# Performance work log

Measured on AMD Instinct MI355X. Metric: run time of the kernel, lower is better.

Reference implementation:

```python
import jax, jax.numpy as jnp
import numpy as np

N_USER, N_TX, E = 50000, 50000, 600000
D_USER, D_TX, D_ALIGN, HID, OUT = 128, 64, 128, 256, 128


def setup_inputs() -> dict:
    key = jax.random.key(0)
    ks = jax.random.split(key, 16)
    s = 0.05
    return {
        "x_user": jax.random.normal(ks[0], (N_USER, D_USER), jnp.float32),
        "x_tx": jax.random.normal(ks[1], (N_TX, D_TX), jnp.float32),
        "edge_user_tx": jax.random.randint(ks[2], (2, E), 0, N_USER),
        "edge_tx_user": jax.random.randint(ks[3], (2, E), 0, N_TX),
        "W_align_user": jax.random.normal(ks[4], (D_USER, D_ALIGN), jnp.float32) * s,
        "b_align_user": jnp.zeros((D_ALIGN,), jnp.float32),
        "W_align_tx": jax.random.normal(ks[5], (D_TX, D_ALIGN), jnp.float32) * s,
        "b_align_tx": jnp.zeros((D_ALIGN,), jnp.float32),
        "eps_ut": jnp.zeros((), jnp.float32),
        "eps_tu": jnp.zeros((), jnp.float32),
        "W1_ut": jax.random.normal(ks[6], (D_TX + D_ALIGN, HID), jnp.float32) * s,
        "b1_ut": jnp.zeros((HID,), jnp.float32),
        "W2_ut": jax.random.normal(ks[7], (HID, OUT), jnp.float32) * s,
        "b2_ut": jnp.zeros((OUT,), jnp.float32),
        "W1_tu": jax.random.normal(ks[8], (D_USER + D_ALIGN, HID), jnp.float32) * s,
        "b1_tu": jnp.zeros((HID,), jnp.float32),
        "W2_tu": jax.random.normal(ks[9], (HID, OUT), jnp.float32) * s,
        "b2_tu": jnp.zeros((OUT,), jnp.float32),
    }


def _mlp(h, W1, b1, W2, b2):
    return jnp.maximum(h @ W1 + b1, 0.0) @ W2 + b2


def _hexgin_conv(x_src, x_dst, edge_index, W_a, b_a, eps, W1, b1, W2, b2):
    # align src features, gather along edges, scatter-sum into dst nodes
    a_src = x_src @ W_a + b_a                       # [N_src, D_ALIGN]
    msgs = a_src[edge_index[0]]                     # [E, D_ALIGN] gather
    agg = jax.ops.segment_sum(msgs, edge_index[1], num_segments=x_dst.shape[0])
    h = jnp.concatenate([(1.0 + eps) * x_dst, agg], axis=1)
    return _mlp(h, W1, b1, W2, b2)


def reference(x_user, x_tx, edge_user_tx, edge_tx_user,
              W_align_user, b_align_user, W_align_tx, b_align_tx,
              eps_ut, eps_tu,
              W1_ut, b1_ut, W2_ut, b2_ut,
              W1_tu, b1_tu, W2_tu, b2_tu):
    # relation (user, makes, tx): updates tx nodes
    out_tx = _hexgin_conv(x_user, x_tx, edge_user_tx,
                          W_align_user, b_align_user, eps_ut,
                          W1_ut, b1_ut, W2_ut, b2_ut)
    # relation (tx, to, user): updates user nodes
    out_user = _hexgin_conv(x_tx, x_user, edge_tx_user,
                            W_align_tx, b_align_tx, eps_tu,
                            W1_tu, b1_tu, W2_tu, b2_tu)
    # HeteroConv aggr='sum': single relation per target, so plain outputs
    return out_user, out_tx
```

## Files before the change

kernel.cpp:

```cpp
#include <hip/hip_runtime.h>
#include <hip/hip_bf16.h>


#define D_USER 128
#define D_TX 64
#define D_ALIGN 128
#define HID 256
#define OUT_D 128
#define NNODE 50000
#define BI 32
#define MAXSLOT 62

typedef __attribute__((ext_vector_type(8))) short short8;
typedef __attribute__((ext_vector_type(4))) float f32x4;
typedef unsigned short ush;

__device__ __forceinline__ ush f2bf(float f) {
    union { float f; unsigned u; } v; v.f = f;
    unsigned u = v.u + 0x7fffu + ((v.u >> 16) & 1u);
    return (ush)(u >> 16);
}
__device__ __forceinline__ float2 bfu2f(unsigned u) {
    union { unsigned u; float f; } a, b;
    a.u = (u & 0xffffu) << 16;
    b.u = u & 0xffff0000u;
    return make_float2(a.f, b.f);
}
__device__ __forceinline__ unsigned f2bfu(float2 v) {
    return (unsigned)f2bf(v.x) | ((unsigned)f2bf(v.y) << 16);
}
__device__ __forceinline__ uint4 scale_bf8(uint4 v, float e) {
    unsigned* w = (unsigned*)&v;
    #pragma unroll
    for (int t = 0; t < 4; ++t) {
        float2 f = bfu2f(w[t]);
        w[t] = f2bfu(make_float2(f.x * e, f.y * e));
    }
    return v;
}


__device__ __forceinline__ void dev_fill(const int* __restrict__ e, int E, int i,
                                         int* __restrict__ pad, int dbase)
{
    int d = dbase + e[E + i];
    int s = e[i];
    int pos = atomicAdd(&pad[(size_t)d * BI], 1);
    if (pos < MAXSLOT)
        ((ush*)pad)[(size_t)d * (2 * BI) + 2 + pos] = (ush)s;
}

__device__ __forceinline__ void dev_prep(int b, int tid,
    const float* __restrict__ xu, ush* __restrict__ xbu,
    const float* __restrict__ xt, ush* __restrict__ xbt, int n8u, int n8t,
    const float* __restrict__ Wa_u, const float* __restrict__ ba_u,
    const float* __restrict__ W1_ut,
    const float* __restrict__ Wa_t, const float* __restrict__ ba_t,
    const float* __restrict__ W1_tu,
    const float* __restrict__ W2_ut, const float* __restrict__ W2_tu,
    ush* __restrict__ Bt1a, float* __restrict__ bfv1,
    ush* __restrict__ Bt1b, float* __restrict__ bfv2,
    ush* __restrict__ Bt2a, ush* __restrict__ Bt2b, int gb)
{
    if (b < gb) {
        int i = b * 256 + tid;
        const float* x; ush* xb; int j;
        if (i < n8u) { x = xu; xb = xbu; j = i; }
        else if (i < n8u + n8t) { x = xt; xb = xbt; j = i - n8u; }
        else return;
        const float4 a = *reinterpret_cast<const float4*>(&x[(size_t)j * 8]);
        const float4 c = *reinterpret_cast<const float4*>(&x[(size_t)j * 8 + 4]);
        ush o[8];
        o[0] = f2bf(a.x); o[1] = f2bf(a.y); o[2] = f2bf(a.z); o[3] = f2bf(a.w);
        o[4] = f2bf(c.x); o[5] = f2bf(c.y); o[6] = f2bf(c.z); o[7] = f2bf(c.w);
        *reinterpret_cast<uint4*>(&xb[(size_t)j * 8]) = *reinterpret_cast<uint4*>(o);
        return;
    }
    int idx = (b - gb) * 256 + tid;
    const int KT = 192;
    const int SEG1 = HID * (KT + 1);
    const int SEG2 = OUT_D * HID;
    if (idx < 2 * SEG1) {
        bool r2 = idx >= SEG1;
        int id = r2 ? idx - SEG1 : idx;
        const float* Wa = r2 ? Wa_t : Wa_u;
        const float* ba = r2 ? ba_t : ba_u;
        const float* W1 = r2 ? W1_tu : W1_ut;
        ush* Bt = r2 ? Bt1b : Bt1a;
        float* bfv = r2 ? bfv2 : bfv1;
        const int Dd = r2 ? 128 : 64;
        int c = id & (HID - 1);
        int k = id >> 8;
        const float* w1bot = W1 + (size_t)Dd * HID;
        if (k < Dd) {
            Bt[(size_t)c * KT + k] = f2bf(W1[(size_t)k * HID + c]);
        } else if (k < KT) {
            int ks = k - Dd;
            float acc = 0.f;
            for (int j = 0; j < D_ALIGN; ++j)
                acc += Wa[ks * D_ALIGN + j] * w1bot[(size_t)j * HID + c];
            Bt[(size_t)c * KT + k] = f2bf(acc);
        } else {
            float acc = 0.f;
            for (int j = 0; j < D_ALIGN; ++j)
                acc += ba[j] * w1bot[(size_t)j * HID + c];
            bfv[c] = acc;
        }
    } else if (idx < 2 * SEG1 + 2 * SEG2) {
        int id = idx - 2 * SEG1;
        bool r2 = id >= SEG2;
        if (r2) id -= SEG2;
        const float* W2 = r2 ? W2_tu : W2_ut;
        ush* Bt2 = r2 ? Bt2b : Bt2a;
        int c = id & (OUT_D - 1);
        int k = id >> 7;
        Bt2[(size_t)c * HID + k] = f2bf(W2[(size_t)k * OUT_D + c]);
    }
}

__device__ __forceinline__ int slot_word(const int* blk, int lane)
{
    return ((lane & 31) < 31) ? blk[1 + (lane & 31)] : 0;
}
__device__ __forceinline__ int slot_get(int word, int j)
{
    return (j & 1) ? ((word >> 16) & 0xffff) : (word & 0xffff);
}

__device__ __forceinline__ void dev_agg128(int w, int lane,
    const ush* __restrict__ xbu, const int* __restrict__ pad, ush* __restrict__ Sb1)
{
    const int* blk = pad + (size_t)w * BI;
    const int n = min(blk[0], MAXSLOT);
    const int word = slot_word(blk, lane);
    float2 acc = make_float2(0.f, 0.f);
    int i = 0;
    for (; i + 4 <= n; i += 4) {
        int wa = __shfl(word, i >> 1);
        int wb = __shfl(word, (i >> 1) + 1);
        int s0 = wa & 0xffff, s1 = (wa >> 16) & 0xffff;
        int s2 = wb & 0xffff, s3 = (wb >> 16) & 0xffff;
        unsigned v0 = *reinterpret_cast<const unsigned*>(&xbu[(size_t)s0 * 128 + 2 * lane]);
        unsigned v1 = *reinterpret_cast<const unsigned*>(&xbu[(size_t)s1 * 128 + 2 * lane]);
        unsigned v2 = *reinterpret_cast<const unsigned*>(&xbu[(size_t)s2 * 128 + 2 * lane]);
        unsigned v3 = *reinterpret_cast<const unsigned*>(&xbu[(size_t)s3 * 128 + 2 * lane]);
        float2 f0 = bfu2f(v0), f1 = bfu2f(v1), f2 = bfu2f(v2), f3 = bfu2f(v3);
        acc.x += (f0.x + f1.x) + (f2.x + f3.x);
        acc.y += (f0.y + f1.y) + (f2.y + f3.y);
    }
    for (; i < n; ++i) {
        int ww = __shfl(word, i >> 1);
        int s0 = slot_get(ww, i);
        unsigned v0 = *reinterpret_cast<const unsigned*>(&xbu[(size_t)s0 * 128 + 2 * lane]);
        float2 f0 = bfu2f(v0);
        acc.x += f0.x; acc.y += f0.y;
    }
    *reinterpret_cast<unsigned*>(&Sb1[(size_t)w * 128 + 2 * lane]) = f2bfu(acc);
}

__device__ __forceinline__ void dev_agg64(int w2, int lane,
    const ush* __restrict__ xbt, const int* __restrict__ pad, ush* __restrict__ Sb2)
{
    const int* blk = pad + (size_t)(NNODE + w2) * BI;
    const int n = min(blk[0], MAXSLOT);
    const int word = slot_word(blk, lane);
    const int half = lane >> 5, l2 = lane & 31;
    float2 acc = make_float2(0.f, 0.f);
    int i = 0;
    for (; i + 4 <= n; i += 4) {
        int ja = i + half, jb = i + 2 + half;
        int wa = __shfl(word, ja >> 1);
        int wb = __shfl(word, jb >> 1);
        int s0 = slot_get(wa, ja), s1 = slot_get(wb, jb);
        unsigned v0 = *reinterpret_cast<const unsigned*>(&xbt[(size_t)s0 * 64 + 2 * l2]);
        unsigned v1 = *reinterpret_cast<const unsigned*>(&xbt[(size_t)s1 * 64 + 2 * l2]);
        float2 f0 = bfu2f(v0), f1 = bfu2f(v1);
        acc.x += f0.x + f1.x;
        acc.y += f0.y + f1.y;
    }
    for (; i + 2 <= n; i += 2) {
        int j = i + half;
        int ww = __shfl(word, j >> 1);
        int s0 = slot_get(ww, j);
        unsigned v0 = *reinterpret_cast<const unsigned*>(&xbt[(size_t)s0 * 64 + 2 * l2]);
        float2 f0 = bfu2f(v0);
        acc.x += f0.x; acc.y += f0.y;
    }
    if (i < n && half == 0) {
        int ww = __shfl(word, i >> 1);
        int s0 = slot_get(ww, i);
        unsigned v0 = *reinterpret_cast<const unsigned*>(&xbt[(size_t)s0 * 64 + 2 * l2]);
        float2 f0 = bfu2f(v0);
        acc.x += f0.x; acc.y += f0.y;
    }
    acc.x += __shfl_xor(acc.x, 32);
    acc.y += __shfl_xor(acc.y, 32);
    if (half == 0)
        *reinterpret_cast<unsigned*>(&Sb2[(size_t)w2 * 64 + 2 * l2]) = f2bfu(acc);
}


__global__ __launch_bounds__(256) void kA(
    const int* __restrict__ e_ut, int E, int* __restrict__ pad,
    const float* __restrict__ xu, ush* __restrict__ xbu,
    const float* __restrict__ xt, ush* __restrict__ xbt, int n8u, int n8t,
    const float* __restrict__ Wa_u, const float* __restrict__ ba_u,
    const float* __restrict__ W1_ut,
    const float* __restrict__ Wa_t, const float* __restrict__ ba_t,
    const float* __restrict__ W1_tu,
    const float* __restrict__ W2_ut, const float* __restrict__ W2_tu,
    ush* __restrict__ Bt1a, float* __restrict__ bfv1,
    ush* __restrict__ Bt1b, float* __restrict__ bfv2,
    ush* __restrict__ Bt2a, ush* __restrict__ Bt2b, int gf, int gb)
{
    int b = blockIdx.x, tid = threadIdx.x;
    if (b < gf) {
        int i = b * 256 + tid;
        if (i < E) dev_fill(e_ut, E, i, pad, 0);
    } else {
        dev_prep(b - gf, tid, xu, xbu, xt, xbt, n8u, n8t,
                 Wa_u, ba_u, W1_ut, Wa_t, ba_t, W1_tu, W2_ut, W2_tu,
                 Bt1a, bfv1, Bt1b, bfv2, Bt2a, Bt2b, gb);
    }
}

__global__ __launch_bounds__(256) void kB(
    const int* __restrict__ e_tu, int E, int* __restrict__ pad,
    const ush* __restrict__ xbu, ush* __restrict__ Sb1, int gf)
{
    int b = blockIdx.x, tid = threadIdx.x;
    if (b < gf) {
        int i = b * 256 + tid;
        if (i < E) dev_fill(e_tu, E, i, pad, NNODE);
    } else {
        int w = (b - gf) * 4 + (tid >> 6);
        if (w < NNODE) dev_agg128(w, tid & 63, xbu, pad, Sb1);
    }
}

__global__ __launch_bounds__(256) void kC(
    const ush* __restrict__ xbt, const int* __restrict__ pad, ush* __restrict__ Sb2)
{
    int w2 = blockIdx.x * 4 + (threadIdx.x >> 6);
    if (w2 < NNODE) dev_agg64(w2, threadIdx.x & 63, xbt, pad, Sb2);
}

__global__ __launch_bounds__(256) void mlp1_all(
    const ush* __restrict__ xbt, const ush* __restrict__ xbu,
    const ush* __restrict__ Sb1, const ush* __restrict__ Sb2,
    const ush* __restrict__ Bt1a, const ush* __restrict__ Bt1b,
    const float* __restrict__ bfv1, const float* __restrict__ bfv2,
    const float* __restrict__ b1_ut, const float* __restrict__ b1_tu,
    const int* __restrict__ pad,
    const float* __restrict__ eps_ut, const float* __restrict__ eps_tu,
    ush* __restrict__ hidb1, ush* __restrict__ hidb2, int M, int nb1)
{
    const int KT = 192;
    __shared__ ush As[128 * 40];
    __shared__ ush Bs[128 * 40];
    const int tid = threadIdx.x;
    const bool r2 = (int)blockIdx.y >= nb1;
    const int bm = (r2 ? blockIdx.y - nb1 : blockIdx.y) * 128;
    const int bn = blockIdx.x * 128;
    const ush* xdst = r2 ? xbu : xbt;
    const int Dd = r2 ? 128 : 64;
    const ush* Sb = r2 ? Sb2 : Sb1;
    const int Dsrc = r2 ? 64 : 128;
    const ush* Bt = r2 ? Bt1b : Bt1a;
    const float* bfv = r2 ? bfv2 : bfv1;
    const float* b1 = r2 ? b1_tu : b1_ut;
    const int* dgp = pad + (size_t)(r2 ? NNODE : 0) * BI;
    ush* hidb = r2 ? hidb2 : hidb1;
    const float e = 1.f + (r2 ? eps_tu[0] : eps_ut[0]);

    const int lane = tid & 63, wave = tid >> 6;
    const int wm = wave >> 1, wn = wave & 1;
    const int lo = lane & 15, hi = lane >> 4;

    f32x4 acc[4][4];
    #pragma unroll
    for (int m = 0; m < 4; ++m)
        #pragma unroll
        for (int n = 0; n < 4; ++n)
            acc[m][n] = f32x4{0.f, 0.f, 0.f, 0.f};

    for (int k0 = 0; k0 < KT; k0 += 32) {
        const ush* src = (k0 < Dd) ? xdst : Sb;
        const int ld   = (k0 < Dd) ? Dd : Dsrc;
        const int kb   = (k0 < Dd) ? k0 : k0 - Dd;
        const bool scale = (k0 < Dd);
        #pragma unroll
        for (int q = 0; q < 2; ++q) {
            int idx = tid + 256 * q;
            int r = idx >> 2, c8 = idx & 3;
            int gr = bm + r;
            uint4 v = uint4{0u, 0u, 0u, 0u};
            if (gr < M)
                v = *reinterpret_cast<const uint4*>(&src[(size_t)gr * ld + kb + c8 * 8]);
            if (scale) v = scale_bf8(v, e);
            *reinterpret_cast<uint4*>(&As[r * 40 + c8 * 8]) = v;
        }
        #pragma unroll
        for (int q = 0; q < 2; ++q) {
            int idx = tid + 256 * q;
            int c = idx >> 2, ku = idx & 3;
            uint4 v = *reinterpret_cast<const uint4*>(&Bt[(size_t)(bn + c) * KT + k0 + ku * 8]);
            *reinterpret_cast<uint4*>(&Bs[c * 40 + ku * 8]) = v;
        }
        __syncthreads();
        short8 av[4], bv[4];
        #pragma unroll
        for (int m = 0; m < 4; ++m)
            av[m] = *reinterpret_cast<const short8*>(&As[(wm * 64 + m * 16 + lo) * 40 + hi * 8]);
        #pragma unroll
        for (int n = 0; n < 4; ++n)
            bv[n] = *reinterpret_cast<const short8*>(&Bs[(wn * 64 + n * 16 + lo) * 40 + hi * 8]);
        #pragma unroll
        for (int m = 0; m < 4; ++m)
            #pragma unroll
            for (int n = 0; n < 4; ++n)
                acc[m][n] = __builtin_amdgcn_mfma_f32_16x16x32_bf16(av[m], bv[n], acc[m][n], 0, 0, 0);
        __syncthreads();
    }

    float b1v[4], bfl[4]; int gcv[4];
    #pragma unroll
    for (int n = 0; n < 4; ++n) {
        int gc = bn + wn * 64 + n * 16 + lo;
        gcv[n] = gc; b1v[n] = b1[gc]; bfl[n] = bfv[gc];
    }
    #pragma unroll
    for (int m = 0; m < 4; ++m)
        #pragma unroll
        for (int reg = 0; reg < 4; ++reg) {
            int gr = bm + wm * 64 + m * 16 + hi * 4 + reg;
            if (gr >= M) continue;
            float dgv = (float)dgp[(size_t)gr * BI];
            #pragma unroll
            for (int n = 0; n < 4; ++n) {
                float val = acc[m][n][reg] + b1v[n] + dgv * bfl[n];
                hidb[(size_t)gr * HID + gcv[n]] = f2bf(fmaxf(val, 0.f));
            }
        }
}

__global__ __launch_bounds__(256) void mlp2_all(
    const ush* __restrict__ hidb1, const ush* __restrict__ hidb2,
    const ush* __restrict__ Bt2a, const ush* __restrict__ Bt2b,
    const float* __restrict__ b2_ut, const float* __restrict__ b2_tu,
    float* __restrict__ out_tx, float* __restrict__ out_user, int M, int nb1)
{
    const int KT = 256;
    __shared__ ush As[128 * 40];
    __shared__ ush Bs[128 * 40];
    const int tid = threadIdx.x;
    const bool r2 = (int)blockIdx.y >= nb1;
    const int bm = (r2 ? blockIdx.y - nb1 : blockIdx.y) * 128;
    const ush* hidb = r2 ? hidb2 : hidb1;
    const ush* Bt2 = r2 ? Bt2b : Bt2a;
    const float* b2 = r2 ? b2_tu : b2_ut;
    float* out = r2 ? out_user : out_tx;

    const int lane = tid & 63, wave = tid >> 6;
    const int wm = wave >> 1, wn = wave & 1;
    const int lo = lane & 15, hi = lane >> 4;

    f32x4 acc[4][4];
    #pragma unroll
    for (int m = 0; m < 4; ++m)
        #pragma unroll
        for (int n = 0; n < 4; ++n)
            acc[m][n] = f32x4{0.f, 0.f, 0.f, 0.f};

    for (int k0 = 0; k0 < KT; k0 += 32) {
        #pragma unroll
        for (int q = 0; q < 2; ++q) {
            int idx = tid + 256 * q;
            int r = idx >> 2, ku = idx & 3;
            int gr = bm + r;
            uint4 v = uint4{0u, 0u, 0u, 0u};
            if (gr < M)
                v = *reinterpret_cast<const uint4*>(&hidb[(size_t)gr * KT + k0 + ku * 8]);
            *reinterpret_cast<uint4*>(&As[r * 40 + ku * 8]) = v;
        }
        #pragma unroll
        for (int q = 0; q < 2; ++q) {
            int idx = tid + 256 * q;
            int c = idx >> 2, ku = idx & 3;
            uint4 v = *reinterpret_cast<const uint4*>(&Bt2[(size_t)c * KT + k0 + ku * 8]);
            *reinterpret_cast<uint4*>(&Bs[c * 40 + ku * 8]) = v;
        }
        __syncthreads();
        short8 av[4], bv[4];
        #pragma unroll
        for (int m = 0; m < 4; ++m)
            av[m] = *reinterpret_cast<const short8*>(&As[(wm * 64 + m * 16 + lo) * 40 + hi * 8]);
        #pragma unroll
        for (int n = 0; n < 4; ++n)
            bv[n] = *reinterpret_cast<const short8*>(&Bs[(wn * 64 + n * 16 + lo) * 40 + hi * 8]);
        #pragma unroll
        for (int m = 0; m < 4; ++m)
            #pragma unroll
            for (int n = 0; n < 4; ++n)
                acc[m][n] = __builtin_amdgcn_mfma_f32_16x16x32_bf16(av[m], bv[n], acc[m][n], 0, 0, 0);
        __syncthreads();
    }

    float b2v[4]; int gcv[4];
    #pragma unroll
    for (int n = 0; n < 4; ++n) {
        int gc = wn * 64 + n * 16 + lo;
        gcv[n] = gc; b2v[n] = b2[gc];
    }
    #pragma unroll
    for (int m = 0; m < 4; ++m)
        #pragma unroll
        for (int reg = 0; reg < 4; ++reg) {
            int gr = bm + wm * 64 + m * 16 + hi * 4 + reg;
            if (gr >= M) continue;
            #pragma unroll
            for (int n = 0; n < 4; ++n)
                out[(size_t)gr * OUT_D + gcv[n]] = acc[m][n][reg] + b2v[n];
        }
}

extern "C" void kernel_launch(void* const* d_in, const int* in_sizes, int n_in,
                              void* d_out, int out_size, void* d_ws, size_t ws_size,
                              hipStream_t stream)
{
    const float* x_user   = (const float*)d_in[0];
    const float* x_tx     = (const float*)d_in[1];
    const int*   e_ut     = (const int*)d_in[2];
    const int*   e_tu     = (const int*)d_in[3];
    const float* Wa_user  = (const float*)d_in[4];
    const float* ba_user  = (const float*)d_in[5];
    const float* Wa_tx    = (const float*)d_in[6];
    const float* ba_tx    = (const float*)d_in[7];
    const float* eps_ut   = (const float*)d_in[8];
    const float* eps_tu   = (const float*)d_in[9];
    const float* W1_ut    = (const float*)d_in[10];
    const float* b1_ut    = (const float*)d_in[11];
    const float* W2_ut    = (const float*)d_in[12];
    const float* b2_ut    = (const float*)d_in[13];
    const float* W1_tu    = (const float*)d_in[14];
    const float* b1_tu    = (const float*)d_in[15];
    const float* W2_tu    = (const float*)d_in[16];
    const float* b2_tu    = (const float*)d_in[17];

    const int N_user = in_sizes[0] / D_USER;
    const int N_tx   = in_sizes[1] / D_TX;
    const int E      = in_sizes[2] / 2;
    const int NT     = 2 * NNODE;

    float* out_user = (float*)d_out;
    float* out_tx   = (float*)d_out + (size_t)N_user * OUT_D;

    int*   pad   = (int*)d_ws;
    float* fws   = (float*)d_ws;
    ush*   Bt1a  = (ush*)(fws + 3300000);
    ush*   Bt1b  = (ush*)(fws + 3330000);
    ush*   Bt2a  = (ush*)(fws + 3360000);
    ush*   Bt2b  = (ush*)(fws + 3380000);
    float* bfv1  = fws + 3400000;
    float* bfv2  = fws + 3401000;
    ush*   xbu   = (ush*)(fws + 3410000);
    ush*   xbt   = (ush*)(fws + 6700000);
    ush*   Sb1   = (ush*)(fws + 8400000);
    ush*   Sb2   = (ush*)(fws + 11700000);
    ush*   hidb1 = (ush*)(fws + 13400000);
    ush*   hidb2 = (ush*)(fws + 19900000);

    const int threads = 256;
    const int n8u = N_user * D_USER / 8, n8t = N_tx * D_TX / 8;
    const int gf  = (E + 255) / 256;
    const int gb  = (n8u + n8t + 255) / 256;
    const int gw  = (2 * HID * 193 + 2 * OUT_D * HID + 255) / 256;
    const int ga  = (NNODE + 3) / 4;
    const int nb1 = (NNODE + 127) / 128;

    hipMemsetAsync(pad, 0, (size_t)NT * BI * sizeof(int), stream);

    kA<<<gf + gb + gw, threads, 0, stream>>>(
        e_ut, E, pad, x_user, xbu, x_tx, xbt, n8u, n8t,
        Wa_user, ba_user, W1_ut, Wa_tx, ba_tx, W1_tu, W2_ut, W2_tu,
        Bt1a, bfv1, Bt1b, bfv2, Bt2a, Bt2b, gf, gb);

    kB<<<gf + ga, threads, 0, stream>>>(e_tu, E, pad, xbu, Sb1, gf);

    kC<<<ga, threads, 0, stream>>>(xbt, pad, Sb2);

    dim3 g1(2, 2 * nb1);
    mlp1_all<<<g1, threads, 0, stream>>>(
        xbt, xbu, Sb1, Sb2, Bt1a, Bt1b, bfv1, bfv2, b1_ut, b1_tu,
        pad, eps_ut, eps_tu, hidb1, hidb2, NNODE, nb1);

    dim3 g2(1, 2 * nb1);
    mlp2_all<<<g2, threads, 0, stream>>>(
        hidb1, hidb2, Bt2a, Bt2b, b2_ut, b2_tu, out_tx, out_user, NNODE, nb1);
}
```

Baseline: 199.6 us.

## Fuse both MLP GEMM layers into one kernel keeping hidden tile in LDS

Merges the two MLP kernels into a single kernel that computes a 64-row hidden tile (all 256 hidden columns), keeps it in shared memory as bf16, and immediately multiplies by W2. This removes the global write and re-read of the 50000x256 bf16 hidden buffers for both relations and one launch. The GEMM is also transposed so weights become the A operand, which allows vectorized float4 output stores. In exchange each block reloads the full W1 and W2 tiles for only 64 rows, and uses more LDS per block, which may lower occupancy.

```diff
diff --git a/kernel.cpp b/kernel.cpp
--- a/kernel.cpp
+++ b/kernel.cpp
@@ -10,6 +10,7 @@
 #define NNODE 50000
 #define BI 32
 #define MAXSLOT 62
+#define HPAD 264
 
 typedef __attribute__((ext_vector_type(8))) short short8;
 typedef __attribute__((ext_vector_type(4))) float f32x4;
@@ -245,183 +246,153 @@
     if (w2 < NNODE) dev_agg64(w2, threadIdx.x & 63, xbt, pad, Sb2);
 }
 
-__global__ __launch_bounds__(256) void mlp1_all(
+__global__ __launch_bounds__(256) void mlpF(
     const ush* __restrict__ xbt, const ush* __restrict__ xbu,
     const ush* __restrict__ Sb1, const ush* __restrict__ Sb2,
     const ush* __restrict__ Bt1a, const ush* __restrict__ Bt1b,
     const float* __restrict__ bfv1, const float* __restrict__ bfv2,
     const float* __restrict__ b1_ut, const float* __restrict__ b1_tu,
+    const ush* __restrict__ Bt2a, const ush* __restrict__ Bt2b,
+    const float* __restrict__ b2_ut, const float* __restrict__ b2_tu,
     const int* __restrict__ pad,
     const float* __restrict__ eps_ut, const float* __restrict__ eps_tu,
-    ush* __restrict__ hidb1, ush* __restrict__ hidb2, int M, int nb1)
-{
-    const int KT = 192;
-    __shared__ ush As[128 * 40];
-    __shared__ ush Bs[128 * 40];
+    float* __restrict__ out_tx, float* __restrict__ out_user, int M)
+{
+    __shared__ ush As[64 * 40];
+    __shared__ ush Bs[256 * 40];
+    __shared__ ush Hs[64 * HPAD];
+
     const int tid = threadIdx.x;
-    const bool r2 = (int)blockIdx.y >= nb1;
-    const int bm = (r2 ? blockIdx.y - nb1 : blockIdx.y) * 128;
-    const int bn = blockIdx.x * 128;
+    const bool r2 = blockIdx.y != 0;
+    const int bm = blockIdx.x * 64;
     const ush* xdst = r2 ? xbu : xbt;
     const int Dd = r2 ? 128 : 64;
     const ush* Sb = r2 ? Sb2 : Sb1;
     const int Dsrc = r2 ? 64 : 128;
-    const ush* Bt = r2 ? Bt1b : Bt1a;
+    const ush* Bt1 = r2 ? Bt1b : Bt1a;
     const float* bfv = r2 ? bfv2 : bfv1;
     const float* b1 = r2 ? b1_tu : b1_ut;
+    const ush* Bt2 = r2 ? Bt2b : Bt2a;
+    const float* b2 = r2 ? b2_tu : b2_ut;
     const int* dgp = pad + (size_t)(r2 ? NNODE : 0) * BI;
-    ush* hidb = r2 ? hidb2 : hidb1;
+    float* out = r2 ? out_user : out_tx;
     const float e = 1.f + (r2 ? eps_tu[0] : eps_ut[0]);
 
-    const int lane = tid & 63, wave = tid >> 6;
-    const int wm = wave >> 1, wn = wave & 1;
+    const int lane = tid & 63, wn = tid >> 6;
     const int lo = lane & 15, hi = lane >> 4;
 
     f32x4 acc[4][4];
     #pragma unroll
-    for (int m = 0; m < 4; ++m)
-        #pragma unroll
-        for (int n = 0; n < 4; ++n)
-            acc[m][n] = f32x4{0.f, 0.f, 0.f, 0.f};
-
-    for (int k0 = 0; k0 < KT; k0 += 32) {
-        const ush* src = (k0 < Dd) ? xdst : Sb;
-        const int ld   = (k0 < Dd) ? Dd : Dsrc;
-        const int kb   = (k0 < Dd) ? k0 : k0 - Dd;
-        const bool scale = (k0 < Dd);
-        #pragma unroll
-        for (int q = 0; q < 2; ++q) {
-            int idx = tid + 256 * q;
-            int r = idx >> 2, c8 = idx & 3;
+    for (int a = 0; a < 4; ++a)
+        #pragma unroll
+        for (int b = 0; b < 4; ++b)
+            acc[a][b] = f32x4{0.f, 0.f, 0.f, 0.f};
+
+    const int KT1 = 192;
+    for (int k0 = 0; k0 < KT1; k0 += 32) {
+        {
+            int r = tid >> 2, c8 = tid & 3;
             int gr = bm + r;
+            const ush* src; int ld; int kb; bool sc;
+            if (k0 < Dd) { src = xdst; ld = Dd; kb = k0; sc = true; }
+            else         { src = Sb;   ld = Dsrc; kb = k0 - Dd; sc = false; }
             uint4 v = uint4{0u, 0u, 0u, 0u};
             if (gr < M)
                 v = *reinterpret_cast<const uint4*>(&src[(size_t)gr * ld + kb + c8 * 8]);
-            if (scale) v = scale_bf8(v, e);
+            if (sc) v = scale_bf8(v, e);
             *reinterpret_cast<uint4*>(&As[r * 40 + c8 * 8]) = v;
         }
+        #pragma unroll
+        for (int q = 0; q < 4; ++q) {
+            int idx = tid + 256 * q;
+            int c = idx >> 2, ku = idx & 3;
+            uint4 v = *reinterpret_cast<const uint4*>(&Bt1[(size_t)c * KT1 + k0 + ku * 8]);
+            *reinterpret_cast<uint4*>(&Bs[c * 40 + ku * 8]) = v;
+        }
+        __syncthreads();
+        short8 av[4], bv[4];
+        #pragma unroll
+        for (int fi = 0; fi < 4; ++fi)
+            av[fi] = *reinterpret_cast<const short8*>(&Bs[(wn * 64 + fi * 16 + lo) * 40 + hi * 8]);
+        #pragma unroll
+        for (int fj = 0; fj < 4; ++fj)
+            bv[fj] = *reinterpret_cast<const short8*>(&As[(fj * 16 + lo) * 40 + hi * 8]);
+        #pragma unroll
+        for (int fi = 0; fi < 4; ++fi)
+            #pragma unroll
+            for (int fj = 0; fj < 4; ++fj)
+                acc[fi][fj] = __builtin_amdgcn_mfma_f32_16x16x32_bf16(av[fi], bv[fj], acc[fi][fj], 0, 0, 0);
+        __syncthreads();
+    }
+
+    #pragma unroll
+    for (int fi = 0; fi < 4; ++fi) {
+        int colb = wn * 64 + fi * 16 + hi * 4;
+        float4 b1v = *reinterpret_cast<const float4*>(&b1[colb]);
+        float4 bfl = *reinterpret_cast<const float4*>(&bfv[colb]);
+        #pragma unroll
+        for (int fj = 0; fj < 4; ++fj) {
+            int r = fj * 16 + lo;
+            int gr = bm + r;
+            float dgv = (gr < M) ? (float)dgp[(size_t)gr * BI] : 0.f;
+            float v0 = fmaxf(acc[fi][fj][0] + b1v.x + dgv * bfl.x, 0.f);
+            float v1 = fmaxf(acc[fi][fj][1] + b1v.y + dgv * bfl.y, 0.f);
+            float v2 = fmaxf(acc[fi][fj][2] + b1v.z + dgv * bfl.z, 0.f);
+            float v3 = fmaxf(acc[fi][fj][3] + b1v.w + dgv * bfl.w, 0.f);
+            uint2 u;
+            u.x = f2bfu(make_float2(v0, v1));
+            u.y = f2bfu(make_float2(v2, v3));
+            *reinterpret_cast<uint2*>(&Hs[r * HPAD + colb]) = u;
+        }
+    }
+
+    f32x4 acc2[2][4];
+    #pragma unroll
+    for (int a = 0; a < 2; ++a)
+        #pragma unroll
+        for (int b = 0; b < 4; ++b)
+            acc2[a][b] = f32x4{0.f, 0.f, 0.f, 0.f};
+
+    for (int k0 = 0; k0 < HID; k0 += 32) {
         #pragma unroll
         for (int q = 0; q < 2; ++q) {
             int idx = tid + 256 * q;
             int c = idx >> 2, ku = idx & 3;
-            uint4 v = *reinterpret_cast<const uint4*>(&Bt[(size_t)(bn + c) * KT + k0 + ku * 8]);
+            uint4 v = *reinterpret_cast<const uint4*>(&Bt2[(size_t)c * HID + k0 + ku * 8]);
             *reinterpret_cast<uint4*>(&Bs[c * 40 + ku * 8]) = v;
         }
         __syncthreads();
-        short8 av[4], bv[4];
-        #pragma unroll
-        for (int m = 0; m < 4; ++m)
-            av[m] = *reinterpret_cast<const short8*>(&As[(wm * 64 + m * 16 + lo) * 40 + hi * 8]);
-        #pragma unroll
-        for (int n = 0; n < 4; ++n)
-            bv[n] = *reinterpret_cast<const short8*>(&Bs[(wn * 64 + n * 16 + lo) * 40 + hi * 8]);
-        #pragma unroll
-        for (int m = 0; m < 4; ++m)
+        short8 av2[2], bv2[4];
+        #pragma unroll
+        for (int fi = 0; fi < 2; ++fi)
+            av2[fi] = *reinterpret_cast<const short8*>(&Bs[(wn * 32 + fi * 16 + lo) * 40 + hi * 8]);
+        #pragma unroll
+        for (int fj = 0; fj < 4; ++fj)
+            bv2[fj] = *reinterpret_cast<const short8*>(&Hs[(fj * 16 + lo) * HPAD + k0 + hi * 8]);
+        #pragma unroll
+        for (int fi = 0; fi < 2; ++fi)
             #pragma unroll
-            for (int n = 0; n < 4; ++n)
-                acc[m][n] = __builtin_amdgcn_mfma_f32_16x16x32_bf16(av[m], bv[n], acc[m][n], 0, 0, 0);
+            for (int fj = 0; fj < 4; ++fj)
+                acc2[fi][fj] = __builtin_amdgcn_mfma_f32_16x16x32_bf16(av2[fi], bv2[fj], acc2[fi][fj], 0, 0, 0);
         __syncthreads();
     }
 
-    float b1v[4], bfl[4]; int gcv[4];
     #pragma unroll
-    for (int n = 0; n < 4; ++n) {
-        int gc = bn + wn * 64 + n * 16 + lo;
-        gcv[n] = gc; b1v[n] = b1[gc]; bfl[n] = bfv[gc];
-    }
-    #pragma unroll
-    for (int m = 0; m < 4; ++m)
-        #pragma unroll
-        for (int reg = 0; reg < 4; ++reg) {
-            int gr = bm + wm * 64 + m * 16 + hi * 4 + reg;
+    for (int fi = 0; fi < 2; ++fi) {
+        int colb = wn * 32 + fi * 16 + hi * 4;
+        float4 b2v = *reinterpret_cast<const float4*>(&b2[colb]);
+        #pragma unroll
+        for (int fj = 0; fj < 4; ++fj) {
+            int gr = bm + fj * 16 + lo;
             if (gr >= M) continue;
-            float dgv = (float)dgp[(size_t)gr * BI];
-            #pragma unroll
-            for (int n = 0; n < 4; ++n) {
-                float val = acc[m][n][reg] + b1v[n] + dgv * bfl[n];
-                hidb[(size_t)gr * HID + gcv[n]] = f2bf(fmaxf(val, 0.f));
-            }
-        }
-}
-
-__global__ __launch_bounds__(256) void mlp2_all(
-    const ush* __restrict__ hidb1, const ush* __restrict__ hidb2,
-    const ush* __restrict__ Bt2a, const ush* __restrict__ Bt2b,
-    const float* __restrict__ b2_ut, const float* __restrict__ b2_tu,
-    float* __restrict__ out_tx, float* __restrict__ out_user, int M, int nb1)
-{
-    const int KT = 256;
-    __shared__ ush As[128 * 40];
-    __shared__ ush Bs[128 * 40];
-    const int tid = threadIdx.x;
-    const bool r2 = (int)blockIdx.y >= nb1;
-    const int bm = (r2 ? blockIdx.y - nb1 : blockIdx.y) * 128;
-    const ush* hidb = r2 ? hidb2 : hidb1;
-    const ush* Bt2 = r2 ? Bt2b : Bt2a;
-    const float* b2 = r2 ? b2_tu : b2_ut;
-    float* out = r2 ? out_user : out_tx;
-
-    const int lane = tid & 63, wave = tid >> 6;
-    const int wm = wave >> 1, wn = wave & 1;
-    const int lo = lane & 15, hi = lane >> 4;
-
-    f32x4 acc[4][4];
-    #pragma unroll
-    for (int m = 0; m < 4; ++m)
-        #pragma unroll
-        for (int n = 0; n < 4; ++n)
-            acc[m][n] = f32x4{0.f, 0.f, 0.f, 0.f};
-
-    for (int k0 = 0; k0 < KT; k0 += 32) {
-        #pragma unroll
-        for (int q = 0; q < 2; ++q) {
-            int idx = tid + 256 * q;
-            int r = idx >> 2, ku = idx & 3;
-            int gr = bm + r;
-            uint4 v = uint4{0u, 0u, 0u, 0u};
-            if (gr < M)
-                v = *reinterpret_cast<const uint4*>(&hidb[(size_t)gr * KT + k0 + ku * 8]);
-            *reinterpret_cast<uint4*>(&As[r * 40 + ku * 8]) = v;
-        }
-        #pragma unroll
-        for (int q = 0; q < 2; ++q) {
-            int idx = tid + 256 * q;
-            int c = idx >> 2, ku = idx & 3;
-            uint4 v = *reinterpret_cast<const uint4*>(&Bt2[(size_t)c * KT + k0 + ku * 8]);
-            *reinterpret_cast<uint4*>(&Bs[c * 40 + ku * 8]) = v;
-        }
-        __syncthreads();
-        short8 av[4], bv[4];
-        #pragma unroll
-        for (int m = 0; m < 4; ++m)
-            av[m] = *reinterpret_cast<const short8*>(&As[(wm * 64 + m * 16 + lo) * 40 + hi * 8]);
-        #pragma unroll
-        for (int n = 0; n < 4; ++n)
-            bv[n] = *reinterpret_cast<const short8*>(&Bs[(wn * 64 + n * 16 + lo) * 40 + hi * 8]);
-        #pragma unroll
-        for (int m = 0; m < 4; ++m)
-            #pragma unroll
-            for (int n = 0; n < 4; ++n)
-                acc[m][n] = __builtin_amdgcn_mfma_f32_16x16x32_bf16(av[m], bv[n], acc[m][n], 0, 0, 0);
-        __syncthreads();
-    }
-
-    float b2v[4]; int gcv[4];
-    #pragma unroll
-    for (int n = 0; n < 4; ++n) {
-        int gc = wn * 64 + n * 16 + lo;
-        gcv[n] = gc; b2v[n] = b2[gc];
-    }
-    #pragma unroll
-    for (int m = 0; m < 4; ++m)
-        #pragma unroll
-        for (int reg = 0; reg < 4; ++reg) {
-            int gr = bm + wm * 64 + m * 16 + hi * 4 + reg;
-            if (gr >= M) continue;
-            #pragma unroll
-            for (int n = 0; n < 4; ++n)
-                out[(size_t)gr * OUT_D + gcv[n]] = acc[m][n][reg] + b2v[n];
-        }
+            float4 o;
+            o.x = acc2[fi][fj][0] + b2v.x;
+            o.y = acc2[fi][fj][1] + b2v.y;
+            o.z = acc2[fi][fj][2] + b2v.z;
+            o.w = acc2[fi][fj][3] + b2v.w;
+            *reinterpret_cast<float4*>(&out[(size_t)gr * OUT_D + colb]) = o;
+        }
+    }
 }
 
 extern "C" void kernel_launch(void* const* d_in, const int* in_sizes, int n_in,
@@ -467,8 +438,6 @@
     ush*   xbt   = (ush*)(fws + 6700000);
     ush*   Sb1   = (ush*)(fws + 8400000);
     ush*   Sb2   = (ush*)(fws + 11700000);
-    ush*   hidb1 = (ush*)(fws + 13400000);
-    ush*   hidb2 = (ush*)(fws + 19900000);
 
     const int threads = 256;
     const int n8u = N_user * D_USER / 8, n8t = N_tx * D_TX / 8;
@@ -476,7 +445,7 @@
     const int gb  = (n8u + n8t + 255) / 256;
     const int gw  = (2 * HID * 193 + 2 * OUT_D * HID + 255) / 256;
     const int ga  = (NNODE + 3) / 4;
-    const int nb1 = (NNODE + 127) / 128;
+    const int nbF = (NNODE + 63) / 64;
 
     hipMemsetAsync(pad, 0, (size_t)NT * BI * sizeof(int), stream);
 
@@ -489,12 +458,9 @@
 
     kC<<<ga, threads, 0, stream>>>(xbt, pad, Sb2);
 
-    dim3 g1(2, 2 * nb1);
-    mlp1_all<<<g1, threads, 0, stream>>>(
+    dim3 gF(nbF, 2);
+    mlpF<<<gF, threads, 0, stream>>>(
         xbt, xbu, Sb1, Sb2, Bt1a, Bt1b, bfv1, bfv2, b1_ut, b1_tu,
-        pad, eps_ut, eps_tu, hidb1, hidb2, NNODE, nb1);
-
-    dim3 g2(1, 2 * nb1);
-    mlp2_all<<<g2, threads, 0, stream>>>(
-        hidb1, hidb2, Bt2a, Bt2b, b2_ut, b2_tu, out_tx, out_user, NNODE, nb1);
-}
+        Bt2a, Bt2b, b2_ut, b2_tu, pad, eps_ut, eps_tu,
+        out_tx, out_user, NNODE);
+}
```

Result: faster. 187.3 us (-6.1%).

## Split MLP stages per relation and co-schedule mlp1 of one with mlp2 of other

Applied to the files above, without the earlier changes.

Replaces the two combined MLP kernels with three launches: mlp1 for the tx relation, then a kernel that mixes mlp1 for the user relation with mlp2 for the tx relation, then mlp2 for the user relation. The GEMM bodies are factored into device functions. The intent is to mix independent work into one grid to balance tails across stages, at the cost of one extra kernel launch and an extra stage boundary.

```diff
diff --git a/kernel.cpp b/kernel.cpp
--- a/kernel.cpp
+++ b/kernel.cpp
@@ -200,6 +200,155 @@
 }
 
 
+__device__ void dev_mlp1(ush* As, ush* Bs, int tid, int bx, int bm,
+    const ush* __restrict__ xdst, int Dd,
+    const ush* __restrict__ Sb, int Dsrc,
+    const ush* __restrict__ Bt, const float* __restrict__ bfv,
+    const float* __restrict__ b1, const int* __restrict__ dgp,
+    float e, ush* __restrict__ hidb, int M)
+{
+    const int KT = 192;
+    const int bn = bx * 128;
+    const int lane = tid & 63, wave = tid >> 6;
+    const int wm = wave >> 1, wn = wave & 1;
+    const int lo = lane & 15, hi = lane >> 4;
+
+    f32x4 acc[4][4];
+    #pragma unroll
+    for (int m = 0; m < 4; ++m)
+        #pragma unroll
+        for (int n = 0; n < 4; ++n)
+            acc[m][n] = f32x4{0.f, 0.f, 0.f, 0.f};
+
+    for (int k0 = 0; k0 < KT; k0 += 32) {
+        const ush* src = (k0 < Dd) ? xdst : Sb;
+        const int ld   = (k0 < Dd) ? Dd : Dsrc;
+        const int kb   = (k0 < Dd) ? k0 : k0 - Dd;
+        const bool scl = (k0 < Dd);
+        #pragma unroll
+        for (int q = 0; q < 2; ++q) {
+            int idx = tid + 256 * q;
+            int r = idx >> 2, c8 = idx & 3;
+            int gr = bm + r;
+            uint4 v = uint4{0u, 0u, 0u, 0u};
+            if (gr < M)
+                v = *reinterpret_cast<const uint4*>(&src[(size_t)gr * ld + kb + c8 * 8]);
+            if (scl) v = scale_bf8(v, e);
+            *reinterpret_cast<uint4*>(&As[r * 40 + c8 * 8]) = v;
+        }
+        #pragma unroll
+        for (int q = 0; q < 2; ++q) {
+            int idx = tid + 256 * q;
+            int c = idx >> 2, ku = idx & 3;
+            uint4 v = *reinterpret_cast<const uint4*>(&Bt[(size_t)(bn + c) * KT + k0 + ku * 8]);
+            *reinterpret_cast<uint4*>(&Bs[c * 40 + ku * 8]) = v;
+        }
+        __syncthreads();
+        short8 av[4], bv[4];
+        #pragma unroll
+        for (int m = 0; m < 4; ++m)
+            av[m] = *reinterpret_cast<const short8*>(&As[(wm * 64 + m * 16 + lo) * 40 + hi * 8]);
+        #pragma unroll
+        for (int n = 0; n < 4; ++n)
+            bv[n] = *reinterpret_cast<const short8*>(&Bs[(wn * 64 + n * 16 + lo) * 40 + hi * 8]);
+        #pragma unroll
+        for (int m = 0; m < 4; ++m)
+            #pragma unroll
+            for (int n = 0; n < 4; ++n)
+                acc[m][n] = __builtin_amdgcn_mfma_f32_16x16x32_bf16(av[m], bv[n], acc[m][n], 0, 0, 0);
+        __syncthreads();
+    }
+
+    float b1v[4], bfl[4]; int gcv[4];
+    #pragma unroll
+    for (int n = 0; n < 4; ++n) {
+        int gc = bn + wn * 64 + n * 16 + lo;
+        gcv[n] = gc; b1v[n] = b1[gc]; bfl[n] = bfv[gc];
+    }
+    #pragma unroll
+    for (int m = 0; m < 4; ++m)
+        #pragma unroll
+        for (int reg = 0; reg < 4; ++reg) {
+            int gr = bm + wm * 64 + m * 16 + hi * 4 + reg;
+            if (gr >= M) continue;
+            float dgv = (float)dgp[(size_t)gr * BI];
+            #pragma unroll
+            for (int n = 0; n < 4; ++n) {
+                float val = acc[m][n][reg] + b1v[n] + dgv * bfl[n];
+                hidb[(size_t)gr * HID + gcv[n]] = f2bf(fmaxf(val, 0.f));
+            }
+        }
+}
+
+__device__ void dev_mlp2(ush* As, ush* Bs, int tid, int bm,
+    const ush* __restrict__ hidb, const ush* __restrict__ Bt2,
+    const float* __restrict__ b2, float* __restrict__ out, int M)
+{
+    const int KT = 256;
+    const int lane = tid & 63, wave = tid >> 6;
+    const int wm = wave >> 1, wn = wave & 1;
+    const int lo = lane & 15, hi = lane >> 4;
+
+    f32x4 acc[4][4];
+    #pragma unroll
+    for (int m = 0; m < 4; ++m)
+        #pragma unroll
+        for (int n = 0; n < 4; ++n)
+            acc[m][n] = f32x4{0.f, 0.f, 0.f, 0.f};
+
+    for (int k0 = 0; k0 < KT; k0 += 32) {
+        #pragma unroll
+        for (int q = 0; q < 2; ++q) {
+            int idx = tid + 256 * q;
+            int r = idx >> 2, ku = idx & 3;
+            int gr = bm + r;
+            uint4 v = uint4{0u, 0u, 0u, 0u};
+            if (gr < M)
+                v = *reinterpret_cast<const uint4*>(&hidb[(size_t)gr * KT + k0 + ku * 8]);
+            *reinterpret_cast<uint4*>(&As[r * 40 + ku * 8]) = v;
+        }
+        #pragma unroll
+        for (int q = 0; q < 2; ++q) {
+            int idx = tid + 256 * q;
+            int c = idx >> 2, ku = idx & 3;
+            uint4 v = *reinterpret_cast<const uint4*>(&Bt2[(size_t)c * KT + k0 + ku * 8]);
+            *reinterpret_cast<uint4*>(&Bs[c * 40 + ku * 8]) = v;
+        }
+        __syncthreads();
+        short8 av[4], bv[4];
+        #pragma unroll
+        for (int m = 0; m < 4; ++m)
+            av[m] = *reinterpret_cast<const short8*>(&As[(wm * 64 + m * 16 + lo) * 40 + hi * 8]);
+        #pragma unroll
+        for (int n = 0; n < 4; ++n)
+            bv[n] = *reinterpret_cast<const short8*>(&Bs[(wn * 64 + n * 16 + lo) * 40 + hi * 8]);
+        #pragma unroll
+        for (int m = 0; m < 4; ++m)
+            #pragma unroll
+            for (int n = 0; n < 4; ++n)
+                acc[m][n] = __builtin_amdgcn_mfma_f32_16x16x32_bf16(av[m], bv[n], acc[m][n], 0, 0, 0);
+        __syncthreads();
+    }
+
+    float b2v[4]; int gcv[4];
+    #pragma unroll
+    for (int n = 0; n < 4; ++n) {
+        int gc = wn * 64 + n * 16 + lo;
+        gcv[n] = gc; b2v[n] = b2[gc];
+    }
+    #pragma unroll
+    for (int m = 0; m < 4; ++m)
+        #pragma unroll
+        for (int reg = 0; reg < 4; ++reg) {
+            int gr = bm + wm * 64 + m * 16 + hi * 4 + reg;
+            if (gr >= M) continue;
+            #pragma unroll
+            for (int n = 0; n < 4; ++n)
+                out[(size_t)gr * OUT_D + gcv[n]] = acc[m][n][reg] + b2v[n];
+        }
+}
+
+
 __global__ __launch_bounds__(256) void kA(
     const int* __restrict__ e_ut, int E, int* __restrict__ pad,
     const float* __restrict__ xu, ush* __restrict__ xbu,
@@ -245,184 +394,52 @@
     if (w2 < NNODE) dev_agg64(w2, threadIdx.x & 63, xbt, pad, Sb2);
 }
 
-__global__ __launch_bounds__(256) void mlp1_all(
-    const ush* __restrict__ xbt, const ush* __restrict__ xbu,
-    const ush* __restrict__ Sb1, const ush* __restrict__ Sb2,
-    const ush* __restrict__ Bt1a, const ush* __restrict__ Bt1b,
-    const float* __restrict__ bfv1, const float* __restrict__ bfv2,
-    const float* __restrict__ b1_ut, const float* __restrict__ b1_tu,
-    const int* __restrict__ pad,
-    const float* __restrict__ eps_ut, const float* __restrict__ eps_tu,
-    ush* __restrict__ hidb1, ush* __restrict__ hidb2, int M, int nb1)
-{
-    const int KT = 192;
+__global__ __launch_bounds__(256) void kD(
+    const ush* __restrict__ xbt, const ush* __restrict__ Sb1,
+    const ush* __restrict__ Bt1a, const float* __restrict__ bfv1,
+    const float* __restrict__ b1_ut, const int* __restrict__ pad,
+    const float* __restrict__ eps_ut, ush* __restrict__ hidb1, int M)
+{
     __shared__ ush As[128 * 40];
     __shared__ ush Bs[128 * 40];
-    const int tid = threadIdx.x;
-    const bool r2 = (int)blockIdx.y >= nb1;
-    const int bm = (r2 ? blockIdx.y - nb1 : blockIdx.y) * 128;
-    const int bn = blockIdx.x * 128;
-    const ush* xdst = r2 ? xbu : xbt;
-    const int Dd = r2 ? 128 : 64;
-    const ush* Sb = r2 ? Sb2 : Sb1;
-    const int Dsrc = r2 ? 64 : 128;
-    const ush* Bt = r2 ? Bt1b : Bt1a;
-    const float* bfv = r2 ? bfv2 : bfv1;
-    const float* b1 = r2 ? b1_tu : b1_ut;
-    const int* dgp = pad + (size_t)(r2 ? NNODE : 0) * BI;
-    ush* hidb = r2 ? hidb2 : hidb1;
-    const float e = 1.f + (r2 ? eps_tu[0] : eps_ut[0]);
-
-    const int lane = tid & 63, wave = tid >> 6;
-    const int wm = wave >> 1, wn = wave & 1;
-    const int lo = lane & 15, hi = lane >> 4;
-
-    f32x4 acc[4][4];
-    #pragma unroll
-    for (int m = 0; m < 4; ++m)
-        #pragma unroll
-        for (int n = 0; n < 4; ++n)
-            acc[m][n] = f32x4{0.f, 0.f, 0.f, 0.f};
-
-    for (int k0 = 0; k0 < KT; k0 += 32) {
-        const ush* src = (k0 < Dd) ? xdst : Sb;
-        const int ld   = (k0 < Dd) ? Dd : Dsrc;
-        const int kb   = (k0 < Dd) ? k0 : k0 - Dd;
-        const bool scale = (k0 < Dd);
-        #pragma unroll
-        for (int q = 0; q < 2; ++q) {
-            int idx = tid + 256 * q;
-            int r = idx >> 2, c8 = idx & 3;
-            int gr = bm + r;
-            uint4 v = uint4{0u, 0u, 0u, 0u};
-            if (gr < M)
-                v = *reinterpret_cast<const uint4*>(&src[(size_t)gr * ld + kb + c8 * 8]);
-            if (scale) v = scale_bf8(v, e);
-            *reinterpret_cast<uint4*>(&As[r * 40 + c8 * 8]) = v;
-        }
-        #pragma unroll
-        for (int q = 0; q < 2; ++q) {
-            int idx = tid + 256 * q;
-            int c = idx >> 2, ku = idx & 3;
-            uint4 v = *reinterpret_cast<const uint4*>(&Bt[(size_t)(bn + c) * KT + k0 + ku * 8]);
-            *reinterpret_cast<uint4*>(&Bs[c * 40 + ku * 8]) = v;
-        }
-        __syncthreads();
-        short8 av[4], bv[4];
-        #pragma unroll
-        for (int m = 0; m < 4; ++m)
-            av[m] = *reinterpret_cast<const short8*>(&As[(wm * 64 + m * 16 + lo) * 40 + hi * 8]);
-        #pragma unroll
-        for (int n = 0; n < 4; ++n)
-            bv[n] = *reinterpret_cast<const short8*>(&Bs[(wn * 64 + n * 16 + lo) * 40 + hi * 8]);
-        #pragma unroll
-        for (int m = 0; m < 4; ++m)
-            #pragma unroll
-            for (int n = 0; n < 4; ++n)
-                acc[m][n] = __builtin_amdgcn_mfma_f32_16x16x32_bf16(av[m], bv[n], acc[m][n], 0, 0, 0);
-        __syncthreads();
-    }
-
-    float b1v[4], bfl[4]; int gcv[4];
-    #pragma unroll
-    for (int n = 0; n < 4; ++n) {
-        int gc = bn + wn * 64 + n * 16 + lo;
-        gcv[n] = gc; b1v[n] = b1[gc]; bfl[n] = bfv[gc];
-    }
-    #pragma unroll
-    for (int m = 0; m < 4; ++m)
-        #pragma unroll
-        for (int reg = 0; reg < 4; ++reg) {
-            int gr = bm + wm * 64 + m * 16 + hi * 4 + reg;
-            if (gr >= M) continue;
-            float dgv = (float)dgp[(size_t)gr * BI];
-            #pragma unroll
-            for (int n = 0; n < 4; ++n) {
-                float val = acc[m][n][reg] + b1v[n] + dgv * bfl[n];
-                hidb[(size_t)gr * HID + gcv[n]] = f2bf(fmaxf(val, 0.f));
-            }
-        }
-}
-
-__global__ __launch_bounds__(256) void mlp2_all(
-    const ush* __restrict__ hidb1, const ush* __restrict__ hidb2,
-    const ush* __restrict__ Bt2a, const ush* __restrict__ Bt2b,
-    const float* __restrict__ b2_ut, const float* __restrict__ b2_tu,
-    float* __restrict__ out_tx, float* __restrict__ out_user, int M, int nb1)
-{
-    const int KT = 256;
+    int b = blockIdx.x;
+    dev_mlp1(As, Bs, threadIdx.x, b & 1, (b >> 1) * 128,
+             xbt, D_TX, Sb1, D_USER, Bt1a, bfv1, b1_ut, pad,
+             1.f + eps_ut[0], hidb1, M);
+}
+
+__global__ __launch_bounds__(256) void kE(
+    const ush* __restrict__ xbu, const ush* __restrict__ Sb2,
+    const ush* __restrict__ Bt1b, const float* __restrict__ bfv2,
+    const float* __restrict__ b1_tu, const int* __restrict__ pad,
+    const float* __restrict__ eps_tu, ush* __restrict__ hidb2,
+    const ush* __restrict__ hidb1, const ush* __restrict__ Bt2a,
+    const float* __restrict__ b2_ut, float* __restrict__ out_tx,
+    int M, int gm1)
+{
     __shared__ ush As[128 * 40];
     __shared__ ush Bs[128 * 40];
-    const int tid = threadIdx.x;
-    const bool r2 = (int)blockIdx.y >= nb1;
-    const int bm = (r2 ? blockIdx.y - nb1 : blockIdx.y) * 128;
-    const ush* hidb = r2 ? hidb2 : hidb1;
-    const ush* Bt2 = r2 ? Bt2b : Bt2a;
-    const float* b2 = r2 ? b2_tu : b2_ut;
-    float* out = r2 ? out_user : out_tx;
-
-    const int lane = tid & 63, wave = tid >> 6;
-    const int wm = wave >> 1, wn = wave & 1;
-    const int lo = lane & 15, hi = lane >> 4;
-
-    f32x4 acc[4][4];
-    #pragma unroll
-    for (int m = 0; m < 4; ++m)
-        #pragma unroll
-        for (int n = 0; n < 4; ++n)
-            acc[m][n] = f32x4{0.f, 0.f, 0.f, 0.f};
-
-    for (int k0 = 0; k0 < KT; k0 += 32) {
-        #pragma unroll
-        for (int q = 0; q < 2; ++q) {
-            int idx = tid + 256 * q;
-            int r = idx >> 2, ku = idx & 3;
-            int gr = bm + r;
-            uint4 v = uint4{0u, 0u, 0u, 0u};
-            if (gr < M)
-                v = *reinterpret_cast<const uint4*>(&hidb[(size_t)gr * KT + k0 + ku * 8]);
-            *reinterpret_cast<uint4*>(&As[r * 40 + ku * 8]) = v;
-        }
-        #pragma unroll
-        for (int q = 0; q < 2; ++q) {
-            int idx = tid + 256 * q;
-            int c = idx >> 2, ku = idx & 3;
-            uint4 v = *reinterpret_cast<const uint4*>(&Bt2[(size_t)c * KT + k0 + ku * 8]);
-            *reinterpret_cast<uint4*>(&Bs[c * 40 + ku * 8]) = v;
-        }
-        __syncthreads();
-        short8 av[4], bv[4];
-        #pragma unroll
-        for (int m = 0; m < 4; ++m)
-            av[m] = *reinterpret_cast<const short8*>(&As[(wm * 64 + m * 16 + lo) * 40 + hi * 8]);
-        #pragma unroll
-        for (int n = 0; n < 4; ++n)
-            bv[n] = *reinterpret_cast<const short8*>(&Bs[(wn * 64 + n * 16 + lo) * 40 + hi * 8]);
-        #pragma unroll
-        for (int m = 0; m < 4; ++m)
-            #pragma unroll
-            for (int n = 0; n < 4; ++n)
-                acc[m][n] = __builtin_amdgcn_mfma_f32_16x16x32_bf16(av[m], bv[n], acc[m][n], 0, 0, 0);
-        __syncthreads();
-    }
-
-    float b2v[4]; int gcv[4];
-    #pragma unroll
-    for (int n = 0; n < 4; ++n) {
-        int gc = wn * 64 + n * 16 + lo;
-        gcv[n] = gc; b2v[n] = b2[gc];
-    }
-    #pragma unroll
-    for (int m = 0; m < 4; ++m)
-        #pragma unroll
-        for (int reg = 0; reg < 4; ++reg) {
-            int gr = bm + wm * 64 + m * 16 + hi * 4 + reg;
-            if (gr >= M) continue;
-            #pragma unroll
-            for (int n = 0; n < 4; ++n)
-                out[(size_t)gr * OUT_D + gcv[n]] = acc[m][n][reg] + b2v[n];
-        }
-}
+    int b = blockIdx.x;
+    if (b < gm1) {
+        dev_mlp1(As, Bs, threadIdx.x, b & 1, (b >> 1) * 128,
+                 xbu, D_USER, Sb2, D_TX, Bt1b, bfv2, b1_tu,
+                 pad + (size_t)NNODE * BI, 1.f + eps_tu[0], hidb2, M);
+    } else {
+        dev_mlp2(As, Bs, threadIdx.x, (b - gm1) * 128,
+                 hidb1, Bt2a, b2_ut, out_tx, M);
+    }
+}
+
+__global__ __launch_bounds__(256) void kF(
+    const ush* __restrict__ hidb2, const ush* __restrict__ Bt2b,
+    const float* __restrict__ b2_tu, float* __restrict__ out_user, int M)
+{
+    __shared__ ush As[128 * 40];
+    __shared__ ush Bs[128 * 40];
+    dev_mlp2(As, Bs, threadIdx.x, blockIdx.x * 128, hidb2, Bt2b, b2_tu,
+             out_user, M);
+}
+
 
 extern "C" void kernel_launch(void* const* d_in, const int* in_sizes, int n_in,
                               void* d_out, int out_size, void* d_ws, size_t ws_size,
@@ -477,6 +494,7 @@
     const int gw  = (2 * HID * 193 + 2 * OUT_D * HID + 255) / 256;
     const int ga  = (NNODE + 3) / 4;
     const int nb1 = (NNODE + 127) / 128;
+    const int gm1 = 2 * nb1;
 
     hipMemsetAsync(pad, 0, (size_t)NT * BI * sizeof(int), stream);
 
@@ -489,12 +507,12 @@
 
     kC<<<ga, threads, 0, stream>>>(xbt, pad, Sb2);
 
-    dim3 g1(2, 2 * nb1);
-    mlp1_all<<<g1, threads, 0, stream>>>(
-        xbt, xbu, Sb1, Sb2, Bt1a, Bt1b, bfv1, bfv2, b1_ut, b1_tu,
-        pad, eps_ut, eps_tu, hidb1, hidb2, NNODE, nb1);
-
-    dim3 g2(1, 2 * nb1);
-    mlp2_all<<<g2, threads, 0, stream>>>(
-        hidb1, hidb2, Bt2a, Bt2b, b2_ut, b2_tu, out_tx, out_user, NNODE, nb1);
-}
+    kD<<<gm1, threads, 0, stream>>>(
+        xbt, Sb1, Bt1a, bfv1, b1_ut, pad, eps_ut, hidb1, NNODE);
+
+    kE<<<gm1 + nb1, threads, 0, stream>>>(
+        xbu, Sb2, Bt1b, bfv2, b1_tu, pad, eps_tu, hidb2,
+        hidb1, Bt2a, b2_ut, out_tx, NNODE, gm1);
+
+    kF<<<nb1, threads, 0, stream>>>(hidb2, Bt2b, b2_tu, out_user, NNODE);
+}
```

Measured after the change: 264.3 us. 32.4% more time.
